# Performance work log

Hardware: AMD Instinct MI355X
Metric: run time of the kernel (lower is better)

Reference implementation:

```python
import jax, jax.numpy as jnp
import numpy as np

EPS = 1e-6

def layer_norm_2d(x, w, b):
    # channel-first LayerNorm over dim 1 of (B, C, H, W)
    u = x.mean(axis=1, keepdims=True)
    s = ((x - u) ** 2).mean(axis=1, keepdims=True)
    xn = (x - u) / jnp.sqrt(s + EPS)
    return w[None, :, None, None] * xn + b[None, :, None, None]


def setup_inputs() -> dict:
    key = jax.random.key(0)
    ks = jax.random.split(key, 5)
    B, C, H, W = 2, 256, 48, 48
    mem_dim, T = 64, 5
    x = jax.random.normal(ks[0], (B, C, H, W), jnp.float32)
    keys = jax.random.normal(ks[1], (B, mem_dim, T, H, W), jnp.float32)
    vals = jax.random.normal(ks[2], (B, mem_dim, T, H, W), jnp.float32)
    wq = jax.random.normal(ks[3], (mem_dim, C), jnp.float32) * 0.05
    wo = jax.random.normal(ks[4], (C, mem_dim), jnp.float32) * 0.05
    wg = jax.random.normal(jax.random.fold_in(key, 7), (C, 2 * C), jnp.float32) * 0.05
    return {
        "x": x, "keys": keys, "vals": vals,
        "wq": wq, "lnq_w": jnp.ones((mem_dim,), jnp.float32), "lnq_b": jnp.zeros((mem_dim,), jnp.float32),
        "wo": wo, "lno_w": jnp.ones((C,), jnp.float32), "lno_b": jnp.zeros((C,), jnp.float32),
        "wg": wg, "bg": jnp.zeros((C,), jnp.float32),
    }


def reference(x, keys, vals, wq, lnq_w, lnq_b, wo, lno_w, lno_b, wg, bg):
    B, C, H, W = x.shape
    mem_dim = wq.shape[0]
    nh = 4
    hd = mem_dim // nh
    scale = hd ** -0.5

    # query projection: 1x1 conv + LayerNorm2d
    q = jnp.einsum('oc,bchw->bohw', wq, x)            # (B, mem_dim, H, W)
    q = layer_norm_2d(q, lnq_w, lnq_b)
    q = q.reshape(B, mem_dim, H * W).transpose(0, 2, 1)      # (B, HW, mem_dim)
    q = q.reshape(B, H * W, nh, hd).transpose(0, 2, 1, 3)    # (B, nh, HW, hd)

    # memory bank: (B, mem_dim, T, Hm, Wm) -> (B, nh, L, hd)
    _, _, T, Hm, Wm = keys.shape
    L = T * Hm * Wm
    k = keys.transpose(0, 2, 3, 4, 1).reshape(B, L, nh, hd).transpose(0, 2, 1, 3)
    v = vals.transpose(0, 2, 3, 4, 1).reshape(B, L, nh, hd).transpose(0, 2, 1, 3)

    attn = jnp.einsum('bnqd,bnkd->bnqk', q, k) * scale       # (B, nh, HW, L)
    attn = jax.nn.softmax(attn, axis=-1)
    mem = jnp.einsum('bnqk,bnkd->bnqd', attn, v)             # (B, nh, HW, hd)
    mem = mem.transpose(0, 2, 1, 3).reshape(B, H * W, mem_dim)
    mem = mem.transpose(0, 2, 1).reshape(B, mem_dim, H, W)

    # output projection: 1x1 conv + LayerNorm2d
    mem_out = jnp.einsum('om,bmhw->bohw', wo, mem)
    mem_out = layer_norm_2d(mem_out, lno_w, lno_b)

    # sigmoid-gated residual fusion
    cat = jnp.concatenate([x, mem_out], axis=1)              # (B, 2C, H, W)
    gate = jax.nn.sigmoid(jnp.einsum('oc,bchw->bohw', wg, cat) + bg[None, :, None, None])
    return x + gate * mem_out
```

## Files before the change

### kernel.cpp

```cpp
#include <hip/hip_runtime.h>
#include <hip/hip_bf16.h>

#define B_   2
#define C_   256
#define HW_  2304
#define MD_  64
#define NH_  4
#define HD_  16
#define LL_  11520
#define EPS_ 1e-6f

typedef __attribute__((ext_vector_type(8)))  short    short8;
typedef __attribute__((ext_vector_type(16))) float    f32x16;
typedef __attribute__((ext_vector_type(4)))  unsigned u32x4;

__device__ __forceinline__ unsigned pk2(float a, float b) {
  unsigned short lo = __builtin_bit_cast(unsigned short, __float2bfloat16(a));
  unsigned short hi = __builtin_bit_cast(unsigned short, __float2bfloat16(b));
  return (unsigned)lo | ((unsigned)hi << 16);
}

__global__ __launch_bounds__(256) void kT(const float* __restrict__ keys,
                                          const float* __restrict__ vals,
                                          __hip_bfloat16* __restrict__ kt,
                                          __hip_bfloat16* __restrict__ vt)
{
  __shared__ float tile[16][256];
  const int bn = blockIdx.x / 45;
  const int l0 = (blockIdx.x % 45) * 256;
  const int tid = threadIdx.x;
  const float* kbase = keys + (size_t)bn * 16 * LL_ + l0;
  const float* vbase = vals + (size_t)bn * 16 * LL_ + l0;
  __hip_bfloat16* vout = vt + (size_t)bn * 18 * LL_ + l0;
  #pragma unroll
  for (int d = 0; d < 16; ++d) {
    tile[d][tid] = kbase[d * LL_ + tid];
    vout[d * LL_ + tid] = __float2bfloat16(vbase[d * LL_ + tid]);
  }
  vout[16 * LL_ + tid] = __float2bfloat16(1.0f);
  vout[17 * LL_ + tid] = __float2bfloat16(0.0f);
  __syncthreads();
  __hip_bfloat16* ko = kt + ((size_t)bn * LL_ + l0 + tid) * 16;
  u32x4 w0, w1;
  #pragma unroll
  for (int j = 0; j < 4; ++j) w0[j] = pk2(tile[2*j][tid],   tile[2*j+1][tid]);
  #pragma unroll
  for (int j = 0; j < 4; ++j) w1[j] = pk2(tile[8+2*j][tid], tile[8+2*j+1][tid]);
  ((u32x4*)ko)[0] = w0;
  ((u32x4*)ko)[1] = w1;
}

__global__ __launch_bounds__(256) void kW(const float* __restrict__ wo,
                                          const float* __restrict__ wg,
                                          const float* __restrict__ wq,
                                          __hip_bfloat16* __restrict__ wop,
                                          __hip_bfloat16* __restrict__ wgp,
                                          __hip_bfloat16* __restrict__ wqp)
{
  const int tid = threadIdx.x;
  const int unit = blockIdx.x * 4 + (tid >> 6);
  const int l = tid & 63;
  u32x4 wv;
  if (unit < 256) {
    const int t = unit >> 5, ks = unit & 31;
    const float* src = wg + (size_t)(t * 32 + (l & 31)) * 512 + ks * 16 + (l >> 5) * 8;
    #pragma unroll
    for (int j = 0; j < 4; ++j) wv[j] = pk2(src[2*j], src[2*j+1]);
    *(u32x4*)(wgp + ((size_t)unit * 64 + l) * 8) = wv;
  } else if (unit < 288) {
    const int v = unit - 256;
    const int t = v >> 2, ks = v & 3;
    const float* src = wo + (size_t)(t * 32 + (l & 31)) * 64 + ks * 16 + (l >> 5) * 8;
    #pragma unroll
    for (int j = 0; j < 4; ++j) wv[j] = pk2(src[2*j], src[2*j+1]);
    *(u32x4*)(wop + ((size_t)v * 64 + l) * 8) = wv;
  } else {
    const int v = unit - 288;
    const int t = v >> 4, ks = v & 15;
    const float* src = wq + (size_t)(t * 32 + (l & 31)) * 256 + ks * 16 + (l >> 5) * 8;
    #pragma unroll
    for (int j = 0; j < 4; ++j) wv[j] = pk2(src[2*j], src[2*j+1]);
    *(u32x4*)(wqp + ((size_t)v * 64 + l) * 8) = wv;
  }
}

__global__ __launch_bounds__(128) void kA(const float* __restrict__ x,
                                          const __hip_bfloat16* __restrict__ wqp,
                                          const float* __restrict__ lnw,
                                          const float* __restrict__ lnb,
                                          __hip_bfloat16* __restrict__ qb)
{
  __shared__ __align__(16) unsigned char xl[16384];
  __shared__ float red_s[2][32], red_q[2][32];
  __shared__ float lnwl[64], lnbl[64];

  const int tid = threadIdx.x;
  const int pix0 = blockIdx.x * 32;
  const int b = pix0 / HW_, sp0 = pix0 % HW_;

  if (tid < 64) { lnwl[tid] = lnw[tid]; lnbl[tid] = lnb[tid]; }

  #pragma unroll 8
  for (int it = 0; it < 32; ++it) {
    const int u = tid + it * 128;
    const int pix = u & 31, cp = u >> 5;
    const float a0 = x[((size_t)(b * C_ + 2 * cp)) * HW_ + sp0 + pix];
    const float a1 = x[((size_t)(b * C_ + 2 * cp + 1)) * HW_ + sp0 + pix];
    *(unsigned*)(xl + pix * 512 + ((4 * cp) ^ ((pix & 7) << 4))) = pk2(a0, a1);
  }
  __syncthreads();

  const int w = tid >> 6, l = tid & 63, col = l & 31, hi = l >> 5;
  const int swz = (col & 7) << 4;

  f32x16 acc;
  #pragma unroll
  for (int i = 0; i < 16; ++i) acc[i] = 0.f;
  #pragma unroll
  for (int ks = 0; ks < 16; ++ks) {
    const u32x4 af = *(const u32x4*)(wqp + ((size_t)((w * 16 + ks) * 64 + l)) * 8);
    const u32x4 bf = *(const u32x4*)(xl + col * 512 + (((ks * 16 + hi * 8) * 2) ^ swz));
    acc = __builtin_amdgcn_mfma_f32_32x32x16_bf16(
        __builtin_bit_cast(short8, af), __builtin_bit_cast(short8, bf), acc, 0, 0, 0);
  }

  float s = 0.f, q = 0.f;
  #pragma unroll
  for (int r = 0; r < 16; ++r) { s += acc[r]; q += acc[r] * acc[r]; }
  s += __shfl_xor(s, 32);
  q += __shfl_xor(q, 32);
  if (hi == 0) { red_s[w][col] = s; red_q[w][col] = q; }
  __syncthreads();
  const float su = red_s[0][col] + red_s[1][col];
  const float qu = red_q[0][col] + red_q[1][col];
  const float u_  = su * (1.f / 64.f);
  const float var = qu * (1.f / 64.f) - u_ * u_;
  const float inv = rsqrtf(var + EPS_);
  const float QS  = 0.25f * 1.4426950408889634f;

  #pragma unroll
  for (int r = 0; r < 16; r += 2) {
    const int ch = w * 32 + (r & 3) + 8 * (r >> 2) + 4 * hi;
    const float q0v = (lnwl[ch]   * ((acc[r]   - u_) * inv) + lnbl[ch])   * QS;
    const float q1v = (lnwl[ch+1] * ((acc[r+1] - u_) * inv) + lnbl[ch+1]) * QS;
    const int n = ch >> 4, d = ch & 15;
    *(unsigned*)(qb + ((size_t)(b * NH_ + n) * HW_ + sp0 + col) * 16 + d) = pk2(q0v, q1v);
  }
}

__global__ __launch_bounds__(512, 4) void kB(const __hip_bfloat16* __restrict__ qb,
                                             const __hip_bfloat16* __restrict__ kt,
                                             const __hip_bfloat16* __restrict__ vt,
                                             float* __restrict__ mem)
{
  __shared__ float red[8][32][17];
  const int blk = blockIdx.x;
  const int bn = blk & 7;
  const int qt = blk >> 3;
  const int b = bn >> 2, n = bn & 3;
  const int tid = threadIdx.x;
  const int wv = tid >> 6;
  const int l  = tid & 63;
  const int col = l & 31;
  const int hi  = l >> 5;
  const int q0 = qt * 32;

  const u32x4 qf = *(const u32x4*)(qb + ((size_t)bn * HW_ + q0 + col) * 16 + hi * 8);
  const short8 qv = __builtin_bit_cast(short8, qf);

  const __hip_bfloat16* pK = kt + ((size_t)bn * LL_ + col) * 16 + hi * 8;
  const int d2 = (col < 17) ? col : 17;
  const __hip_bfloat16* pV = vt + ((size_t)(bn * 18 + d2)) * LL_ + hi * 8;

  f32x16 acc;
  #pragma unroll
  for (int i = 0; i < 16; ++i) acc[i] = 0.f;

  const int kbeg = wv * 1440;

  u32x4 kc = *(const u32x4*)(pK + (size_t)kbeg * 16);
  u32x4 va = *(const u32x4*)(pV + kbeg);
  u32x4 vb = *(const u32x4*)(pV + kbeg + 16);

  for (int t = 0; t < 45; ++t) {
    const int l0 = kbeg + t * 32;
    const int ln = (t < 44) ? (l0 + 32) : kbeg;
    u32x4 kn  = *(const u32x4*)(pK + (size_t)ln * 16);
    u32x4 van = *(const u32x4*)(pV + ln);
    u32x4 vbn = *(const u32x4*)(pV + ln + 16);

    f32x16 s;
    #pragma unroll
    for (int i = 0; i < 16; ++i) s[i] = 0.f;
    s = __builtin_amdgcn_mfma_f32_32x32x16_bf16(__builtin_bit_cast(short8, kc), qv, s, 0, 0, 0);

    float pt[16];
    #pragma unroll
    for (int i = 0; i < 16; ++i) pt[i] = __builtin_amdgcn_exp2f(s[i]);

    {
      unsigned p0 = pk2(pt[0], pt[1]), p1 = pk2(pt[2], pt[3]);
      unsigned p2 = pk2(pt[4], pt[5]), p3 = pk2(pt[6], pt[7]);
      asm volatile("v_permlane32_swap_b32 %0, %1" : "+v"(p0), "+v"(p2));
      asm volatile("v_permlane32_swap_b32 %0, %1" : "+v"(p1), "+v"(p3));
      u32x4 pa; pa[0] = p0; pa[1] = p1; pa[2] = p2; pa[3] = p3;
      acc = __builtin_amdgcn_mfma_f32_32x32x16_bf16(
          __builtin_bit_cast(short8, pa), __builtin_bit_cast(short8, va), acc, 0, 0, 0);
    }
    {
      unsigned p0 = pk2(pt[8],  pt[9]),  p1 = pk2(pt[10], pt[11]);
      unsigned p2 = pk2(pt[12], pt[13]), p3 = pk2(pt[14], pt[15]);
      asm volatile("v_permlane32_swap_b32 %0, %1" : "+v"(p0), "+v"(p2));
      asm volatile("v_permlane32_swap_b32 %0, %1" : "+v"(p1), "+v"(p3));
      u32x4 pa; pa[0] = p0; pa[1] = p1; pa[2] = p2; pa[3] = p3;
      acc = __builtin_amdgcn_mfma_f32_32x32x16_bf16(
          __builtin_bit_cast(short8, pa), __builtin_bit_cast(short8, vb), acc, 0, 0, 0);
    }
    kc = kn; va = van; vb = vbn;
  }

  if (col <= 16) {
    #pragma unroll
    for (int r = 0; r < 16; ++r) {
      const int row = (r & 3) + 8 * (r >> 2) + 4 * hi;
      red[wv][row][col] = acc[r];
    }
  }
  __syncthreads();
  {
    const int row = tid >> 4, c = tid & 15;
    float num = 0.f, den = 0.f;
    #pragma unroll
    for (int ww = 0; ww < 8; ++ww) {
      num += red[ww][row][c];
      den += red[ww][row][16];
    }
    mem[((size_t)b * HW_ + q0 + row) * MD_ + n * HD_ + c] = num / den;
  }
}

__global__ __launch_bounds__(512) void kC(const float* __restrict__ x,
                                          const float* __restrict__ mem,
                                          const __hip_bfloat16* __restrict__ wop,
                                          const __hip_bfloat16* __restrict__ wgp,
                                          const float* __restrict__ lnw,
                                          const float* __restrict__ lnb,
                                          const float* __restrict__ bg,
                                          float* __restrict__ out)
{
  __shared__ __align__(16) unsigned char xl[16384];
  __shared__ __align__(16) unsigned char mol[16384];
  __shared__ __align__(16) unsigned char ml[4096];
  __shared__ float red_s[8][32], red_q[8][32];
  __shared__ float lnwl[256], lnbl[256], bgl[256];

  const int tid = threadIdx.x;
  const int pix0 = blockIdx.x * 32;
  const int b = pix0 / HW_, sp0 = pix0 % HW_;

  if (tid < 256) { lnwl[tid] = lnw[tid]; lnbl[tid] = lnb[tid]; bgl[tid] = bg[tid]; }

  #pragma unroll
  for (int it = 0; it < 8; ++it) {
    const int u = tid + it * 512;
    const int pix = u & 31, cp = u >> 5;
    const float a0 = x[((size_t)(b * C_ + 2 * cp)) * HW_ + sp0 + pix];
    const float a1 = x[((size_t)(b * C_ + 2 * cp + 1)) * HW_ + sp0 + pix];
    *(unsigned*)(xl + pix * 512 + ((4 * cp) ^ ((pix & 7) << 4))) = pk2(a0, a1);
  }
  #pragma unroll
  for (int it = 0; it < 2; ++it) {
    const int u = tid + it * 512;
    const int mp = u & 31, pix = u >> 5;
    const float2 m2 = *(const float2*)(mem + ((size_t)(b * HW_ + sp0 + pix)) * MD_ + 2 * mp);
    *(unsigned*)(ml + pix * 128 + ((4 * mp) ^ ((pix & 7) << 4))) = pk2(m2.x, m2.y);
  }
  __syncthreads();

  const int w = tid >> 6, l = tid & 63, col = l & 31, hi = l >> 5;
  const int swz = (col & 7) << 4;

  f32x16 acc;
  #pragma unroll
  for (int i = 0; i < 16; ++i) acc[i] = 0.f;
  #pragma unroll
  for (int ks = 0; ks < 4; ++ks) {
    const u32x4 af = *(const u32x4*)(wop + ((size_t)((w * 4 + ks) * 64 + l)) * 8);
    const u32x4 bf = *(const u32x4*)(ml + col * 128 + (((ks * 16 + hi * 8) * 2) ^ swz));
    acc = __builtin_amdgcn_mfma_f32_32x32x16_bf16(
        __builtin_bit_cast(short8, af), __builtin_bit_cast(short8, bf), acc, 0, 0, 0);
  }

  float s = 0.f, q = 0.f;
  #pragma unroll
  for (int r = 0; r < 16; ++r) { s += acc[r]; q += acc[r] * acc[r]; }
  s += __shfl_xor(s, 32);
  q += __shfl_xor(q, 32);
  if (hi == 0) { red_s[w][col] = s; red_q[w][col] = q; }
  __syncthreads();
  float su = 0.f, qu = 0.f;
  #pragma unroll
  for (int ww = 0; ww < 8; ++ww) { su += red_s[ww][col]; qu += red_q[ww][col]; }
  const float u_  = su * (1.f / 256.f);
  const float var = qu * (1.f / 256.f) - u_ * u_;
  const float inv = rsqrtf(var + EPS_);

  float moln[16];
  #pragma unroll
  for (int r = 0; r < 16; ++r) {
    const int ch = w * 32 + (r & 3) + 8 * (r >> 2) + 4 * hi;
    moln[r] = lnwl[ch] * ((acc[r] - u_) * inv) + lnbl[ch];
  }
  #pragma unroll
  for (int r = 0; r < 16; r += 2) {
    const int ch = w * 32 + (r & 3) + 8 * (r >> 2) + 4 * hi;
    *(unsigned*)(mol + col * 512 + ((2 * ch) ^ swz)) = pk2(moln[r], moln[r + 1]);
  }
  __syncthreads();

  f32x16 acc2;
  #pragma unroll
  for (int i = 0; i < 16; ++i) acc2[i] = 0.f;
  #pragma unroll
  for (int ks = 0; ks < 16; ++ks) {
    const u32x4 af = *(const u32x4*)(wgp + ((size_t)((w * 32 + ks) * 64 + l)) * 8);
    const u32x4 bf = *(const u32x4*)(xl + col * 512 + (((ks * 16 + hi * 8) * 2) ^ swz));
    acc2 = __builtin_amdgcn_mfma_f32_32x32x16_bf16(
        __builtin_bit_cast(short8, af), __builtin_bit_cast(short8, bf), acc2, 0, 0, 0);
  }
  #pragma unroll
  for (int ks = 0; ks < 16; ++ks) {
    const u32x4 af = *(const u32x4*)(wgp + ((size_t)((w * 32 + 16 + ks) * 64 + l)) * 8);
    const u32x4 bf = *(const u32x4*)(mol + col * 512 + (((ks * 16 + hi * 8) * 2) ^ swz));
    acc2 = __builtin_amdgcn_mfma_f32_32x32x16_bf16(
        __builtin_bit_cast(short8, af), __builtin_bit_cast(short8, bf), acc2, 0, 0, 0);
  }

  #pragma unroll
  for (int r = 0; r < 16; ++r) {
    const int ch = w * 32 + (r & 3) + 8 * (r >> 2) + 4 * hi;
    const size_t idx = ((size_t)(b * C_ + ch)) * HW_ + sp0 + col;
    const float z = acc2[r] + bgl[ch];
    const float gate = 1.f / (1.f + __expf(-z));
    out[idx] = x[idx] + gate * moln[r];
  }
}

extern "C" void kernel_launch(void* const* d_in, const int* in_sizes, int n_in,
                              void* d_out, int out_size, void* d_ws, size_t ws_size,
                              hipStream_t stream)
{
  const float* x    = (const float*)d_in[0];
  const float* keys = (const float*)d_in[1];
  const float* vals = (const float*)d_in[2];
  const float* wq   = (const float*)d_in[3];
  const float* lnqw = (const float*)d_in[4];
  const float* lnqb = (const float*)d_in[5];
  const float* wo   = (const float*)d_in[6];
  const float* lnow = (const float*)d_in[7];
  const float* lnob = (const float*)d_in[8];
  const float* wg   = (const float*)d_in[9];
  const float* bg   = (const float*)d_in[10];
  float* out = (float*)d_out;

  __hip_bfloat16* qbf = (__hip_bfloat16*)d_ws;
  __hip_bfloat16* kt  = qbf + (size_t)B_ * NH_ * HW_ * HD_;
  __hip_bfloat16* vt  = kt + (size_t)B_ * NH_ * LL_ * HD_;
  __hip_bfloat16* wgp = vt + (size_t)B_ * NH_ * 18 * LL_;
  __hip_bfloat16* wop = wgp + (size_t)256 * 64 * 8;
  __hip_bfloat16* wqp = wop + (size_t)32 * 64 * 8;
  float* memws = (float*)(wqp + (size_t)32 * 64 * 8);

  kT<<<360, 256, 0, stream>>>(keys, vals, kt, vt);
  kW<<<80, 256, 0, stream>>>(wo, wg, wq, wop, wgp, wqp);
  kA<<<144, 128, 0, stream>>>(x, wqp, lnqw, lnqb, qbf);
  kB<<<576, 512, 0, stream>>>(qbf, kt, vt, memws);
  kC<<<144, 512, 0, stream>>>(x, memws, wop, wgp, lnow, lnob, bg, out);
}
```

Baseline: 153.8 us.

## Split attention key range across two blocks and combine partial sums in output kernel

The attention kernel now launches twice as many 256-thread blocks, each covering half of the key range with four waves, and writes unnormalized numerator and denominator partials to separate workspace halves. The output-projection kernel sums the two halves and divides while loading mem into shared memory. The aim is better scheduling granularity and occupancy on the attention stage. The cost is extra global traffic for the partials and slightly more work in the consumer. The combine relies on a fixed exponent offset, so partial sums stay consistent across splits.

```diff
diff --git a/kernel.cpp b/kernel.cpp
--- a/kernel.cpp
+++ b/kernel.cpp
@@ -9,6 +9,8 @@
 #define HD_  16
 #define LL_  11520
 #define EPS_ 1e-6f
+#define NUMSZ (B_ * HW_ * MD_)
+#define DENSZ (B_ * HW_ * 4)
 
 typedef __attribute__((ext_vector_type(8)))  short    short8;
 typedef __attribute__((ext_vector_type(16))) float    f32x16;
@@ -148,15 +150,17 @@
   }
 }
 
-__global__ __launch_bounds__(512, 4) void kB(const __hip_bfloat16* __restrict__ qb,
-                                             const __hip_bfloat16* __restrict__ kt,
-                                             const __hip_bfloat16* __restrict__ vt,
-                                             float* __restrict__ mem)
-{
-  __shared__ float red[8][32][17];
+__global__ __launch_bounds__(256) void kB(const __hip_bfloat16* __restrict__ qb,
+                                          const __hip_bfloat16* __restrict__ kt,
+                                          const __hip_bfloat16* __restrict__ vt,
+                                          float* __restrict__ num,
+                                          float* __restrict__ den)
+{
+  __shared__ float red[4][32][17];
   const int blk = blockIdx.x;
   const int bn = blk & 7;
-  const int qt = blk >> 3;
+  const int qt = (blk >> 3) % 72;
+  const int h  = blk / 576;
   const int b = bn >> 2, n = bn & 3;
   const int tid = threadIdx.x;
   const int wv = tid >> 6;
@@ -176,7 +180,7 @@
   #pragma unroll
   for (int i = 0; i < 16; ++i) acc[i] = 0.f;
 
-  const int kbeg = wv * 1440;
+  const int kbeg = (h * 4 + wv) * 1440;
 
   u32x4 kc = *(const u32x4*)(pK + (size_t)kbeg * 16);
   u32x4 va = *(const u32x4*)(pV + kbeg);
@@ -227,20 +231,23 @@
     }
   }
   __syncthreads();
-  {
-    const int row = tid >> 4, c = tid & 15;
-    float num = 0.f, den = 0.f;
-    #pragma unroll
-    for (int ww = 0; ww < 8; ++ww) {
-      num += red[ww][row][c];
-      den += red[ww][row][16];
-    }
-    mem[((size_t)b * HW_ + q0 + row) * MD_ + n * HD_ + c] = num / den;
+  float* numh = num + (size_t)h * NUMSZ;
+  float* denh = den + (size_t)h * DENSZ;
+  #pragma unroll
+  for (int idx = tid; idx < 512; idx += 256) {
+    const int row = idx >> 4, c = idx & 15;
+    numh[((size_t)b * HW_ + q0 + row) * MD_ + n * HD_ + c] =
+        red[0][row][c] + red[1][row][c] + red[2][row][c] + red[3][row][c];
+  }
+  if (tid < 32) {
+    denh[((size_t)b * HW_ + q0 + tid) * 4 + n] =
+        red[0][tid][16] + red[1][tid][16] + red[2][tid][16] + red[3][tid][16];
   }
 }
 
 __global__ __launch_bounds__(512) void kC(const float* __restrict__ x,
-                                          const float* __restrict__ mem,
+                                          const float* __restrict__ num,
+                                          const float* __restrict__ den,
                                           const __hip_bfloat16* __restrict__ wop,
                                           const __hip_bfloat16* __restrict__ wgp,
                                           const float* __restrict__ lnw,
@@ -272,8 +279,13 @@
   for (int it = 0; it < 2; ++it) {
     const int u = tid + it * 512;
     const int mp = u & 31, pix = u >> 5;
-    const float2 m2 = *(const float2*)(mem + ((size_t)(b * HW_ + sp0 + pix)) * MD_ + 2 * mp);
-    *(unsigned*)(ml + pix * 128 + ((4 * mp) ^ ((pix & 7) << 4))) = pk2(m2.x, m2.y);
+    const size_t base = ((size_t)(b * HW_ + sp0 + pix)) * MD_ + 2 * mp;
+    const float2 a0 = *(const float2*)(num + base);
+    const float2 a1 = *(const float2*)(num + NUMSZ + base);
+    const size_t di = ((size_t)(b * HW_ + sp0 + pix)) * 4 + (mp >> 3);
+    const float r = 1.f / (den[di] + den[DENSZ + di]);
+    *(unsigned*)(ml + pix * 128 + ((4 * mp) ^ ((pix & 7) << 4))) =
+        pk2((a0.x + a1.x) * r, (a0.y + a1.y) * r);
   }
   __syncthreads();
 
@@ -369,11 +381,12 @@
   __hip_bfloat16* wgp = vt + (size_t)B_ * NH_ * 18 * LL_;
   __hip_bfloat16* wop = wgp + (size_t)256 * 64 * 8;
   __hip_bfloat16* wqp = wop + (size_t)32 * 64 * 8;
-  float* memws = (float*)(wqp + (size_t)32 * 64 * 8);
+  float* numws = (float*)(wqp + (size_t)32 * 64 * 8);
+  float* denws = numws + 2 * (size_t)NUMSZ;
 
   kT<<<360, 256, 0, stream>>>(keys, vals, kt, vt);
   kW<<<80, 256, 0, stream>>>(wo, wg, wq, wop, wgp, wqp);
   kA<<<144, 128, 0, stream>>>(x, wqp, lnqw, lnqb, qbf);
-  kB<<<576, 512, 0, stream>>>(qbf, kt, vt, memws);
-  kC<<<144, 512, 0, stream>>>(x, memws, wop, wgp, lnow, lnob, bg, out);
-}
+  kB<<<1152, 256, 0, stream>>>(qbf, kt, vt, numws, denws);
+  kC<<<144, 512, 0, stream>>>(x, numws, denws, wop, wgp, lnow, lnob, bg, out);
+}
```

Result: faster. 149.4 us (-2.9%).
